# Kernel tuning notes

Hardware: AMD Instinct MI355X
Metric: run time of the kernel (lower is better)

Reference implementation:

```python
import jax, jax.numpy as jnp
import numpy as np

DIM = 384
NUM_HEADS = 12
WS = 7  # window_size
N = WS * WS
BW = 4096  # batch * num_windows


def _relative_position_index(ws: int) -> np.ndarray:
    coords = np.stack(np.meshgrid(np.arange(ws), np.arange(ws), indexing='ij'))  # [2, ws, ws]
    cf = coords.reshape(2, -1)  # [2, ws*ws]
    rel = cf[:, :, None] - cf[:, None, :]  # [2, N, N]
    rel = rel.transpose(1, 2, 0)
    rel[:, :, 0] += ws - 1
    rel[:, :, 1] += ws - 1
    rel[:, :, 0] *= 2 * ws - 1
    return rel.sum(-1).astype(np.int32)  # [N, N]


def setup_inputs() -> dict:
    key = jax.random.key(0)
    ks = jax.random.split(key, 7)
    x = jax.random.normal(ks[0], (BW, N, DIM), dtype=jnp.float32)
    qkv_w = jax.random.normal(ks[1], (3 * DIM, DIM), dtype=jnp.float32) * 0.02
    qkv_b = jnp.zeros((3 * DIM,), dtype=jnp.float32)
    proj_w = jax.random.normal(ks[2], (DIM, DIM), dtype=jnp.float32) * 0.02
    proj_b = jnp.zeros((DIM,), dtype=jnp.float32)
    rpb_table = jax.random.normal(ks[3], ((2 * WS - 1) ** 2, NUM_HEADS), dtype=jnp.float32) * 0.02
    rel_idx = jnp.asarray(_relative_position_index(WS))
    return {"x": x, "qkv_w": qkv_w, "qkv_b": qkv_b, "proj_w": proj_w,
            "proj_b": proj_b, "rpb_table": rpb_table, "rel_idx": rel_idx}


def reference(x, qkv_w, qkv_b, proj_w, proj_b, rpb_table, rel_idx):
    B, n, C = x.shape
    hd = C // NUM_HEADS
    scale = hd ** (-0.5)
    # QKV projection: [B, N, 3C] -> [3, B, H, N, hd]
    qkv = (x @ qkv_w.T + qkv_b).reshape(B, n, 3, NUM_HEADS, hd).transpose(2, 0, 3, 1, 4)
    q, k, v = qkv[0], qkv[1], qkv[2]
    attn = jnp.einsum('bhnd,bhmd->bhnm', q * scale, k)  # [B, H, N, N]
    # relative position bias gather: [N*N, H] -> [H, N, N]
    bias = rpb_table[rel_idx.reshape(-1)].reshape(n, n, NUM_HEADS).transpose(2, 0, 1)
    attn = jax.nn.softmax(attn + bias[None], axis=-1)
    out = jnp.einsum('bhnm,bhmd->bhnd', attn, v).transpose(0, 2, 1, 3).reshape(B, n, C)
    return out @ proj_w.T + proj_b
```

## Files before the change

kernel.cpp:

```cpp
#include <hip/hip_runtime.h>
#include <hip/hip_bf16.h>

typedef __bf16 bf16_t;
typedef __bf16 bf16x8 __attribute__((ext_vector_type(8)));
typedef __bf16 bf16x4 __attribute__((ext_vector_type(4)));
typedef float  f32x4  __attribute__((ext_vector_type(4)));

#define WBT_OFF   0
#define PWB_OFF   (72*12*512*2)
#define BIASL_OFF (PWB_OFF + 24*12*512*2)
#define QKVB_OFF  (BIASL_OFF + 12*4*4*64*4*4)

#define L_HEAD   49152
#define L_HSTR   23040
#define L_O      141312
#define L_TOT    158720

__global__ void prep_kernel(const float* __restrict__ qkv_w,
                            const float* __restrict__ qkv_b,
                            const float* __restrict__ proj_w,
                            const float* __restrict__ rpb,
                            const int*   __restrict__ rel_idx,
                            char* __restrict__ ws)
{
    const int n_wbf  = 72*12*512;
    const int n_pwf  = 24*12*512;
    const int n_bias = 12*4*4*64*4;
    const int n_qb   = 1152;
    int idx = blockIdx.x * blockDim.x + threadIdx.x;
    if (idx < n_wbf) {
        int j = idx & 7, lane = (idx >> 3) & 63;
        int t = idx >> 9;
        int kk = t % 12, ntile = t / 12;
        int lo = lane & 15, hi = lane >> 4;
        int h = ntile / 6, tct = ntile % 6, s = tct >> 1, db = (tct & 1) << 4;
        ((bf16_t*)(ws + WBT_OFF))[idx] =
            (bf16_t)qkv_w[(s*384 + h*32 + db + lo)*384 + kk*32 + hi*8 + j];
    } else if (idx < n_wbf + n_pwf) {
        int li = idx - n_wbf;
        int j = li & 7, lane = (li >> 3) & 63;
        int t = li >> 9;
        int kk = t % 12, ntile = t / 12;
        int lo = lane & 15, hi = lane >> 4;
        ((bf16_t*)(ws + PWB_OFF))[li] =
            (bf16_t)proj_w[(ntile*16 + lo)*384 + kk*32 + hi*8 + j];
    } else if (idx < n_wbf + n_pwf + n_bias) {
        int li = idx - n_wbf - n_pwf;
        int r  = li & 3;
        int l  = (li >> 2) & 63;
        int ct = (li >> 8) & 3;
        int m  = (li >> 10) & 3;
        int h  = li >> 12;
        int i  = m*16 + ((l >> 4) << 2) + r;
        int jj = ct*16 + (l & 15);
        float v;
        if (jj >= 49)     v = -1e30f;
        else if (i < 49)  v = rpb[rel_idx[i*49 + jj]*12 + h];
        else              v = 0.f;
        ((float*)(ws + BIASL_OFF))[li] = v;
    } else if (idx < n_wbf + n_pwf + n_bias + n_qb) {
        int i = idx - n_wbf - n_pwf - n_bias;
        int h = i / 96, c = i % 96;
        int s = c >> 5, cc = c & 31;
        ((float*)(ws + QKVB_OFF))[i] = qkv_b[s*384 + h*32 + cc];
    }
}

__launch_bounds__(512, 2)
__global__ void fused_attn_kernel(const float* __restrict__ x,
                                  const float* __restrict__ proj_b,
                                  const char*  __restrict__ ws,
                                  float* __restrict__ out)
{
    __shared__ __attribute__((aligned(16))) char smem[L_TOT];

    const int tid = threadIdx.x;
    const int lane = tid & 63, lo = lane & 15, hi = lane >> 4;
    const int w = tid >> 6;
    const int wi = blockIdx.x;

    auto xs_addr = [&](int row, int kb) { return row*768 + (kb ^ ((row & 7) << 4)); };

    uint4 z4 = make_uint4(0u,0u,0u,0u);
    for (int c = tid; c < 15*48; c += 512) {
        int row = 49 + c/48, kc = c%48;
        *(uint4*)(smem + xs_addr(row, kc*16)) = z4;
    }
    const float* xw = x + (size_t)wi * (49*384);
    for (int c = tid; c < 49*48; c += 512) {
        int row = c/48, kc = c%48;
        float4 f0 = *(const float4*)(xw + row*384 + kc*8);
        float4 f1 = *(const float4*)(xw + row*384 + kc*8 + 4);
        bf16x8 t;
        t[0]=(bf16_t)f0.x; t[1]=(bf16_t)f0.y; t[2]=(bf16_t)f0.z; t[3]=(bf16_t)f0.w;
        t[4]=(bf16_t)f1.x; t[5]=(bf16_t)f1.y; t[6]=(bf16_t)f1.z; t[7]=(bf16_t)f1.w;
        *(bf16x8*)(smem + xs_addr(row, kc*16)) = t;
    }
    __syncthreads();

    const bf16_t* WBF   = (const bf16_t*)(ws + WBT_OFF);
    const bf16_t* PWF   = (const bf16_t*)(ws + PWB_OFF);
    const float*  biasQ = (const float*)(ws + QKVB_OFF);
    const float scale = 0.17677669529663687f;
    const f32x4 zz = {0.f,0.f,0.f,0.f};

    f32x4 accP[4][3];
#pragma unroll
    for (int m = 0; m < 4; ++m)
#pragma unroll
        for (int nt = 0; nt < 3; ++nt) accP[m][nt] = zz;

    const int hl_a = w >> 1;
    const int mh   = w & 1;
    char* HA = smem + L_HEAD + hl_a*L_HSTR;

#pragma unroll 1
    for (int pass = 0; pass < 3; ++pass) {
        {
            const bf16_t* bb = WBF + (size_t)(pass*8 + w)*(3*12*512) + (lane << 3);
            f32x4 acc[4][3];
#pragma unroll
            for (int m = 0; m < 4; ++m)
#pragma unroll
                for (int nt = 0; nt < 3; ++nt) acc[m][nt] = zz;

            bf16x8 br[3][3];
#pragma unroll
            for (int k = 0; k < 2; ++k)
#pragma unroll
                for (int nt = 0; nt < 3; ++nt)
                    br[k][nt] = *(const bf16x8*)(bb + ((nt*12 + k) << 9));

#pragma unroll
            for (int kk = 0; kk < 12; ++kk) {
                if (kk < 10) {
#pragma unroll
                    for (int nt = 0; nt < 3; ++nt)
                        br[(kk+2)%3][nt] = *(const bf16x8*)(bb + ((nt*12 + kk+2) << 9));
                }
                bf16x8 a[4];
#pragma unroll
                for (int m = 0; m < 4; ++m)
                    a[m] = *(const bf16x8*)(smem + xs_addr(m*16 + lo, kk*64 + hi*16));
#pragma unroll
                for (int nt = 0; nt < 3; ++nt)
#pragma unroll
                    for (int m = 0; m < 4; ++m)
                        acc[m][nt] = __builtin_amdgcn_mfma_f32_16x16x32_bf16(a[m], br[kk%3][nt], acc[m][nt], 0,0,0);
            }

#pragma unroll
            for (int nt = 0; nt < 3; ++nt) {
                const int ntl = w*3 + nt;
                const int hl = ntl / 6, tct = ntl % 6;
                const int s = tct >> 1, db = (tct & 1) << 4;
                float bq = biasQ[(pass*24 + ntl)*16 + lo];
                char* hb = smem + L_HEAD + hl*L_HSTR;
                if (s == 0) {
#pragma unroll
                    for (int m = 0; m < 4; ++m)
#pragma unroll
                        for (int r = 0; r < 4; ++r)
                            *(bf16_t*)(hb + (m*16 + hi*4 + r)*72 + (db + lo)*2) =
                                (bf16_t)((acc[m][nt][r] + bq) * scale);
                } else if (s == 1) {
#pragma unroll
                    for (int m = 0; m < 4; ++m)
#pragma unroll
                        for (int r = 0; r < 4; ++r)
                            *(bf16_t*)(hb + 4608 + (m*16 + hi*4 + r)*72 + (db + lo)*2) =
                                (bf16_t)(acc[m][nt][r] + bq);
                } else {
#pragma unroll
                    for (int m = 0; m < 4; ++m) {
                        bf16x4 p;
#pragma unroll
                        for (int r = 0; r < 4; ++r) p[r] = (bf16_t)(acc[m][nt][r] + bq);
                        *(bf16x4*)(hb + 9216 + (db + lo)*144 + (m*16 + hi*4)*2) = p;
                    }
                }
            }
        }
        __syncthreads();

        {
            const char* QS = HA;
            const char* KS = HA + 4608;
            const char* VT = HA + 9216;
            char*       P  = HA + 13824;
            const float4* bL = (const float4*)(ws + BIASL_OFF) + (size_t)(pass*4 + hl_a)*1024;

            bf16x8 aq[2], bk[4];
#pragma unroll
            for (int mi = 0; mi < 2; ++mi)
                aq[mi] = *(const bf16x8*)(QS + ((mh*2 + mi)*16 + lo)*72 + hi*16);
#pragma unroll
            for (int ct = 0; ct < 4; ++ct)
                bk[ct] = *(const bf16x8*)(KS + (ct*16 + lo)*72 + hi*16);

#pragma unroll
            for (int mi = 0; mi < 2; ++mi) {
                const int m = mh*2 + mi;
                f32x4 s[4];
#pragma unroll
                for (int ct = 0; ct < 4; ++ct) {
                    s[ct] = __builtin_amdgcn_mfma_f32_16x16x32_bf16(aq[mi], bk[ct], zz, 0,0,0);
                    float4 bv = bL[(m*4 + ct)*64 + lane];
                    s[ct][0]+=bv.x; s[ct][1]+=bv.y; s[ct][2]+=bv.z; s[ct][3]+=bv.w;
                }
#pragma unroll
                for (int r = 0; r < 4; ++r) {
                    float mx = fmaxf(fmaxf(s[0][r],s[1][r]), fmaxf(s[2][r],s[3][r]));
#pragma unroll
                    for (int off = 1; off < 16; off <<= 1) mx = fmaxf(mx, __shfl_xor(mx, off));
                    float e0 = __expf(s[0][r]-mx), e1 = __expf(s[1][r]-mx);
                    float e2 = __expf(s[2][r]-mx), e3 = __expf(s[3][r]-mx);
                    float sum = e0+e1+e2+e3;
#pragma unroll
                    for (int off = 1; off < 16; off <<= 1) sum += __shfl_xor(sum, off);
                    float rinv = 1.0f / sum;
                    int row = m*16 + hi*4 + r;
                    *(bf16_t*)(P + row*144 + (0*16+lo)*2) = (bf16_t)(e0*rinv);
                    *(bf16_t*)(P + row*144 + (1*16+lo)*2) = (bf16_t)(e1*rinv);
                    *(bf16_t*)(P + row*144 + (2*16+lo)*2) = (bf16_t)(e2*rinv);
                    *(bf16_t*)(P + row*144 + (3*16+lo)*2) = (bf16_t)(e3*rinv);
                }
            }
            asm volatile("s_waitcnt lgkmcnt(0)" ::: "memory");

#pragma unroll
            for (int mi = 0; mi < 2; ++mi) {
                const int m = mh*2 + mi;
#pragma unroll
                for (int dt = 0; dt < 2; ++dt) {
                    f32x4 o = zz;
#pragma unroll
                    for (int ks = 0; ks < 2; ++ks) {
                        bf16x8 ap = *(const bf16x8*)(P  + (m*16+lo)*144 + ks*64 + hi*16);
                        bf16x8 bv = *(const bf16x8*)(VT + (dt*16+lo)*144 + ks*64 + hi*16);
                        o = __builtin_amdgcn_mfma_f32_16x16x32_bf16(ap, bv, o, 0,0,0);
                    }
                    const int c2 = (hl_a*32 + dt*16 + lo)*2;
#pragma unroll
                    for (int r = 0; r < 4; ++r)
                        *(bf16_t*)(smem + L_O + (m*16 + hi*4 + r)*272 + c2) = (bf16_t)o[r];
                }
            }
        }
        __syncthreads();

        {
            bf16x8 bp[2][3];
#pragma unroll
            for (int nt = 0; nt < 3; ++nt)
                bp[0][nt] = *(const bf16x8*)(PWF + (size_t)(((w*3 + nt)*12 + pass*4) << 9) + (lane << 3));
#pragma unroll
            for (int kk2 = 0; kk2 < 4; ++kk2) {
                if (kk2 < 3) {
#pragma unroll
                    for (int nt = 0; nt < 3; ++nt)
                        bp[(kk2+1)&1][nt] = *(const bf16x8*)(PWF + (size_t)(((w*3 + nt)*12 + pass*4 + kk2+1) << 9) + (lane << 3));
                }
                bf16x8 ao[4];
#pragma unroll
                for (int m = 0; m < 4; ++m)
                    ao[m] = *(const bf16x8*)(smem + L_O + (m*16 + lo)*272 + kk2*64 + hi*16);
#pragma unroll
                for (int nt = 0; nt < 3; ++nt)
#pragma unroll
                    for (int m = 0; m < 4; ++m)
                        accP[m][nt] = __builtin_amdgcn_mfma_f32_16x16x32_bf16(ao[m], bp[kk2&1][nt], accP[m][nt], 0,0,0);
            }
        }
        __syncthreads();
    }

    float* ow = out + (size_t)wi * (49*384);
#pragma unroll
    for (int nt = 0; nt < 3; ++nt) {
        int cc = (w*3 + nt)*16 + lo;
        float pb = proj_b[cc];
#pragma unroll
        for (int m = 0; m < 4; ++m)
#pragma unroll
            for (int r = 0; r < 4; ++r) {
                int row = m*16 + hi*4 + r;
                if (row < 49) ow[row*384 + cc] = accP[m][nt][r] + pb;
            }
    }
}

extern "C" void kernel_launch(void* const* d_in, const int* in_sizes, int n_in,
                              void* d_out, int out_size, void* d_ws, size_t ws_size,
                              hipStream_t stream)
{
    const float* x      = (const float*)d_in[0];
    const float* qkv_w  = (const float*)d_in[1];
    const float* qkv_b  = (const float*)d_in[2];
    const float* proj_w = (const float*)d_in[3];
    const float* proj_b = (const float*)d_in[4];
    const float* rpb    = (const float*)d_in[5];
    const int*   rel_idx= (const int*)d_in[6];
    char* ws = (char*)d_ws;

    const int total = 72*12*512 + 24*12*512 + 12*4*4*64*4 + 1152;
    prep_kernel<<<(total + 255)/256, 256, 0, stream>>>(qkv_w, qkv_b, proj_w, rpb, rel_idx, ws);
    fused_attn_kernel<<<4096, 512, 0, stream>>>(x, proj_b, ws, (float*)d_out);
}
```

Measured before the change: 702.4 us.

## Keep Q and P in registers via transposed MFMA and pipeline proj across passes

Each warp now computes Q, K and V for its own head half with transposed MFMA operands. Q and the softmax probabilities stay in registers and are rearranged with lane shuffles, so they no longer make a round trip through LDS. The output projection for a pass is deferred into the next pass's attention phase with a double-buffered O tile, which removes one block barrier per pass. The aim is to cut LDS traffic and synchronization, at the cost of redundant Q projection work between the paired warps and more register pressure.

Measured after the change: 934.9 us. 33.1% more time.

```diff
diff --git a/kernel.cpp b/kernel.cpp
--- a/kernel.cpp
+++ b/kernel.cpp
@@ -6,18 +6,17 @@
 typedef __bf16 bf16x4 __attribute__((ext_vector_type(4)));
 typedef float  f32x4  __attribute__((ext_vector_type(4)));
 
+#define MFMA __builtin_amdgcn_mfma_f32_16x16x32_bf16
+
 #define WBT_OFF   0
 #define PWB_OFF   (72*12*512*2)
 #define BIASL_OFF (PWB_OFF + 24*12*512*2)
-#define QKVB_OFF  (BIASL_OFF + 12*4*4*64*4*4)
-
-#define L_HEAD   49152
-#define L_HSTR   23040
-#define L_O      141312
-#define L_TOT    158720
+
+#define L_KV   49152
+#define L_OB   (L_KV + 4*9216)
+#define L_TOT  (L_OB + 2*17408)
 
 __global__ void prep_kernel(const float* __restrict__ qkv_w,
-                            const float* __restrict__ qkv_b,
                             const float* __restrict__ proj_w,
                             const float* __restrict__ rpb,
                             const int*   __restrict__ rel_idx,
@@ -26,7 +25,6 @@
     const int n_wbf  = 72*12*512;
     const int n_pwf  = 24*12*512;
     const int n_bias = 12*4*4*64*4;
-    const int n_qb   = 1152;
     int idx = blockIdx.x * blockDim.x + threadIdx.x;
     if (idx < n_wbf) {
         int j = idx & 7, lane = (idx >> 3) & 63;
@@ -48,35 +46,39 @@
         int li = idx - n_wbf - n_pwf;
         int r  = li & 3;
         int l  = (li >> 2) & 63;
-        int ct = (li >> 8) & 3;
-        int m  = (li >> 10) & 3;
+        int kt = (li >> 8) & 3;
+        int mq = (li >> 10) & 3;
         int h  = li >> 12;
-        int i  = m*16 + ((l >> 4) << 2) + r;
-        int jj = ct*16 + (l & 15);
-        float v;
-        if (jj >= 49)     v = -1e30f;
-        else if (i < 49)  v = rpb[rel_idx[i*49 + jj]*12 + h];
-        else              v = 0.f;
+        int q  = mq*16 + (l & 15);
+        int k  = kt*16 + (l >> 4)*4 + r;
+        float v = (k < 49 && q < 49) ? rpb[rel_idx[q*49 + k]*12 + h] : -1e30f;
         ((float*)(ws + BIASL_OFF))[li] = v;
-    } else if (idx < n_wbf + n_pwf + n_bias + n_qb) {
-        int i = idx - n_wbf - n_pwf - n_bias;
-        int h = i / 96, c = i % 96;
-        int s = c >> 5, cc = c & 31;
-        ((float*)(ws + QKVB_OFF))[i] = qkv_b[s*384 + h*32 + cc];
     }
 }
 
+static __device__ __forceinline__ unsigned pack2(float a, float b) {
+    bf16_t xa = (bf16_t)a, xb = (bf16_t)b;
+    unsigned short ua = __builtin_bit_cast(unsigned short, xa);
+    unsigned short ub = __builtin_bit_cast(unsigned short, xb);
+    return (unsigned)ua | ((unsigned)ub << 16);
+}
+
+union U8 { unsigned u[4]; bf16x8 v; };
+
 __launch_bounds__(512, 2)
-__global__ void fused_attn_kernel(const float* __restrict__ x,
-                                  const float* __restrict__ proj_b,
-                                  const char*  __restrict__ ws,
-                                  float* __restrict__ out)
+__global__ void fused2_kernel(const float* __restrict__ x,
+                              const float* __restrict__ qkv_b,
+                              const float* __restrict__ proj_b,
+                              const char*  __restrict__ ws,
+                              float* __restrict__ out)
 {
     __shared__ __attribute__((aligned(16))) char smem[L_TOT];
 
     const int tid = threadIdx.x;
     const int lane = tid & 63, lo = lane & 15, hi = lane >> 4;
     const int w = tid >> 6;
+    const int hl = w >> 1;
+    const int mh = w & 1;
     const int wi = blockIdx.x;
 
     auto xs_addr = [&](int row, int kb) { return row*768 + (kb ^ ((row & 7) << 4)); };
@@ -98,11 +100,12 @@
     }
     __syncthreads();
 
-    const bf16_t* WBF   = (const bf16_t*)(ws + WBT_OFF);
-    const bf16_t* PWF   = (const bf16_t*)(ws + PWB_OFF);
-    const float*  biasQ = (const float*)(ws + QKVB_OFF);
+    const bf16_t* WBF = (const bf16_t*)(ws + WBT_OFF);
+    const bf16_t* PWF = (const bf16_t*)(ws + PWB_OFF);
+    const float4* bT  = (const float4*)(ws + BIASL_OFF);
     const float scale = 0.17677669529663687f;
     const f32x4 zz = {0.f,0.f,0.f,0.f};
+    const int sb = lo + ((hi & 1) << 5);
 
     f32x4 accP[4][3];
 #pragma unroll
@@ -110,169 +113,218 @@
 #pragma unroll
         for (int nt = 0; nt < 3; ++nt) accP[m][nt] = zz;
 
-    const int hl_a = w >> 1;
-    const int mh   = w & 1;
-    char* HA = smem + L_HEAD + hl_a*L_HSTR;
+    bf16x8 bq[2];
 
 #pragma unroll 1
     for (int pass = 0; pass < 3; ++pass) {
+        const int h = pass*4 + hl;
+
         {
-            const bf16_t* bb = WBF + (size_t)(pass*8 + w)*(3*12*512) + (lane << 3);
-            f32x4 acc[4][3];
-#pragma unroll
-            for (int m = 0; m < 4; ++m)
-#pragma unroll
-                for (int nt = 0; nt < 3; ++nt) acc[m][nt] = zz;
-
-            bf16x8 br[3][3];
-#pragma unroll
-            for (int k = 0; k < 2; ++k)
-#pragma unroll
-                for (int nt = 0; nt < 3; ++nt)
-                    br[k][nt] = *(const bf16x8*)(bb + ((nt*12 + k) << 9));
-
+            const bf16_t* wq0b = WBF + (size_t)((h*6 + 0   )*12)*512 + (lane<<3);
+            const bf16_t* wq1b = WBF + (size_t)((h*6 + 1   )*12)*512 + (lane<<3);
+            const bf16_t* wkb  = WBF + (size_t)((h*6 + 2+mh)*12)*512 + (lane<<3);
+            const bf16_t* wvb  = WBF + (size_t)((h*6 + 4+mh)*12)*512 + (lane<<3);
+
+            f32x4 aq[2][2], ak4[4], av4[4];
+#pragma unroll
+            for (int i = 0; i < 2; ++i) { aq[i][0] = zz; aq[i][1] = zz; }
+#pragma unroll
+            for (int i = 0; i < 4; ++i) { ak4[i] = zz; av4[i] = zz; }
+
+            bf16x8 rq0[3], rq1[3], rk[3], rv[3];
+#pragma unroll
+            for (int t = 0; t < 3; ++t) {
+                rq0[t] = *(const bf16x8*)(wq0b + (t<<9));
+                rq1[t] = *(const bf16x8*)(wq1b + (t<<9));
+                rk [t] = *(const bf16x8*)(wkb  + (t<<9));
+                rv [t] = *(const bf16x8*)(wvb  + (t<<9));
+            }
 #pragma unroll
             for (int kk = 0; kk < 12; ++kk) {
-                if (kk < 10) {
-#pragma unroll
-                    for (int nt = 0; nt < 3; ++nt)
-                        br[(kk+2)%3][nt] = *(const bf16x8*)(bb + ((nt*12 + kk+2) << 9));
-                }
-                bf16x8 a[4];
-#pragma unroll
-                for (int m = 0; m < 4; ++m)
-                    a[m] = *(const bf16x8*)(smem + xs_addr(m*16 + lo, kk*64 + hi*16));
-#pragma unroll
-                for (int nt = 0; nt < 3; ++nt)
-#pragma unroll
-                    for (int m = 0; m < 4; ++m)
-                        acc[m][nt] = __builtin_amdgcn_mfma_f32_16x16x32_bf16(a[m], br[kk%3][nt], acc[m][nt], 0,0,0);
-            }
-
-#pragma unroll
-            for (int nt = 0; nt < 3; ++nt) {
-                const int ntl = w*3 + nt;
-                const int hl = ntl / 6, tct = ntl % 6;
-                const int s = tct >> 1, db = (tct & 1) << 4;
-                float bq = biasQ[(pass*24 + ntl)*16 + lo];
-                char* hb = smem + L_HEAD + hl*L_HSTR;
-                if (s == 0) {
-#pragma unroll
-                    for (int m = 0; m < 4; ++m)
-#pragma unroll
-                        for (int r = 0; r < 4; ++r)
-                            *(bf16_t*)(hb + (m*16 + hi*4 + r)*72 + (db + lo)*2) =
-                                (bf16_t)((acc[m][nt][r] + bq) * scale);
-                } else if (s == 1) {
-#pragma unroll
-                    for (int m = 0; m < 4; ++m)
-#pragma unroll
-                        for (int r = 0; r < 4; ++r)
-                            *(bf16_t*)(hb + 4608 + (m*16 + hi*4 + r)*72 + (db + lo)*2) =
-                                (bf16_t)(acc[m][nt][r] + bq);
-                } else {
-#pragma unroll
-                    for (int m = 0; m < 4; ++m) {
-                        bf16x4 p;
-#pragma unroll
-                        for (int r = 0; r < 4; ++r) p[r] = (bf16_t)(acc[m][nt][r] + bq);
-                        *(bf16x4*)(hb + 9216 + (db + lo)*144 + (m*16 + hi*4)*2) = p;
-                    }
-                }
+                const int sl = kk % 3;
+                bf16x8 xf[4];
+#pragma unroll
+                for (int tt = 0; tt < 4; ++tt)
+                    xf[tt] = *(const bf16x8*)(smem + xs_addr(tt*16 + lo, kk*64 + hi*16));
+#pragma unroll
+                for (int mi = 0; mi < 2; ++mi) {
+                    aq[0][mi] = MFMA(rq0[sl], xf[2*mh + mi], aq[0][mi], 0,0,0);
+                    aq[1][mi] = MFMA(rq1[sl], xf[2*mh + mi], aq[1][mi], 0,0,0);
+                }
+#pragma unroll
+                for (int tt = 0; tt < 4; ++tt) ak4[tt] = MFMA(rk[sl], xf[tt], ak4[tt], 0,0,0);
+#pragma unroll
+                for (int tt = 0; tt < 4; ++tt) av4[tt] = MFMA(xf[tt], rv[sl], av4[tt], 0,0,0);
+                if (kk < 9) {
+                    rq0[sl] = *(const bf16x8*)(wq0b + ((kk+3)<<9));
+                    rq1[sl] = *(const bf16x8*)(wq1b + ((kk+3)<<9));
+                    rk [sl] = *(const bf16x8*)(wkb  + ((kk+3)<<9));
+                    rv [sl] = *(const bf16x8*)(wvb  + ((kk+3)<<9));
+                }
+            }
+
+            float4 qb0 = *(const float4*)(qkv_b + h*32 +      hi*4);
+            float4 qb1 = *(const float4*)(qkv_b + h*32 + 16 + hi*4);
+            unsigned pkq[2][2][2];
+#pragma unroll
+            for (int mi = 0; mi < 2; ++mi) {
+                pkq[0][mi][0] = pack2((aq[0][mi][0]+qb0.x)*scale, (aq[0][mi][1]+qb0.y)*scale);
+                pkq[0][mi][1] = pack2((aq[0][mi][2]+qb0.z)*scale, (aq[0][mi][3]+qb0.w)*scale);
+                pkq[1][mi][0] = pack2((aq[1][mi][0]+qb1.x)*scale, (aq[1][mi][1]+qb1.y)*scale);
+                pkq[1][mi][1] = pack2((aq[1][mi][2]+qb1.z)*scale, (aq[1][mi][3]+qb1.w)*scale);
+            }
+#pragma unroll
+            for (int mi = 0; mi < 2; ++mi) {
+                U8 u;
+#pragma unroll
+                for (int jp = 0; jp < 4; ++jp) {
+                    const int rp = jp & 1, hf = jp >> 1;
+                    const int srcl = sb + (hf << 4);
+                    unsigned s0 = (unsigned)__shfl((int)pkq[0][mi][rp], srcl, 64);
+                    unsigned s1 = (unsigned)__shfl((int)pkq[1][mi][rp], srcl, 64);
+                    u.u[jp] = (hi >> 1) ? s1 : s0;
+                }
+                bq[mi] = u.v;
+            }
+
+            float4 kb = *(const float4*)(qkv_b + 384 + h*32 + mh*16 + hi*4);
+            char* Kl = smem + L_KV + hl*9216;
+#pragma unroll
+            for (int tt = 0; tt < 4; ++tt) {
+                bf16x4 t;
+                t[0]=(bf16_t)(ak4[tt][0]+kb.x); t[1]=(bf16_t)(ak4[tt][1]+kb.y);
+                t[2]=(bf16_t)(ak4[tt][2]+kb.z); t[3]=(bf16_t)(ak4[tt][3]+kb.w);
+                *(bf16x4*)(Kl + (tt*16+lo)*72 + (mh*16+hi*4)*2) = t;
+            }
+            float vb = qkv_b[768 + h*32 + mh*16 + lo];
+            char* Vl = Kl + 4608;
+#pragma unroll
+            for (int tt = 0; tt < 4; ++tt) {
+                bf16x4 t;
+                t[0]=(bf16_t)(av4[tt][0]+vb); t[1]=(bf16_t)(av4[tt][1]+vb);
+                t[2]=(bf16_t)(av4[tt][2]+vb); t[3]=(bf16_t)(av4[tt][3]+vb);
+                *(bf16x4*)(Vl + (mh*16+lo)*144 + (tt*16+hi*4)*2) = t;
             }
         }
         __syncthreads();
 
         {
-            const char* QS = HA;
-            const char* KS = HA + 4608;
-            const char* VT = HA + 9216;
-            char*       P  = HA + 13824;
-            const float4* bL = (const float4*)(ws + BIASL_OFF) + (size_t)(pass*4 + hl_a)*1024;
-
-            bf16x8 aq[2], bk[4];
-#pragma unroll
-            for (int mi = 0; mi < 2; ++mi)
-                aq[mi] = *(const bf16x8*)(QS + ((mh*2 + mi)*16 + lo)*72 + hi*16);
-#pragma unroll
-            for (int ct = 0; ct < 4; ++ct)
-                bk[ct] = *(const bf16x8*)(KS + (ct*16 + lo)*72 + hi*16);
-
+            bf16x8 pw[4][3];
+            if (pass > 0) {
+#pragma unroll
+                for (int kk2 = 0; kk2 < 4; ++kk2)
+#pragma unroll
+                    for (int nt = 0; nt < 3; ++nt)
+                        pw[kk2][nt] = *(const bf16x8*)(PWF +
+                            ((size_t)((w*3+nt)*12 + (pass-1)*4 + kk2) << 9) + (lane<<3));
+            }
+
+            const char* Kl = smem + L_KV + hl*9216;
+            const char* Vl = Kl + 4608;
+            bf16x8 akf[4];
+#pragma unroll
+            for (int kt = 0; kt < 4; ++kt)
+                akf[kt] = *(const bf16x8*)(Kl + (kt*16+lo)*72 + hi*16);
+            bf16x8 avf[2][2];
+#pragma unroll
+            for (int dt = 0; dt < 2; ++dt)
+#pragma unroll
+                for (int ks = 0; ks < 2; ++ks)
+                    avf[dt][ks] = *(const bf16x8*)(Vl + (dt*16+lo)*144 + ks*64 + hi*16);
+
+            char* Ob = smem + L_OB + (pass & 1)*17408;
 #pragma unroll
             for (int mi = 0; mi < 2; ++mi) {
-                const int m = mh*2 + mi;
-                f32x4 s[4];
-#pragma unroll
-                for (int ct = 0; ct < 4; ++ct) {
-                    s[ct] = __builtin_amdgcn_mfma_f32_16x16x32_bf16(aq[mi], bk[ct], zz, 0,0,0);
-                    float4 bv = bL[(m*4 + ct)*64 + lane];
-                    s[ct][0]+=bv.x; s[ct][1]+=bv.y; s[ct][2]+=bv.z; s[ct][3]+=bv.w;
-                }
-#pragma unroll
-                for (int r = 0; r < 4; ++r) {
-                    float mx = fmaxf(fmaxf(s[0][r],s[1][r]), fmaxf(s[2][r],s[3][r]));
-#pragma unroll
-                    for (int off = 1; off < 16; off <<= 1) mx = fmaxf(mx, __shfl_xor(mx, off));
-                    float e0 = __expf(s[0][r]-mx), e1 = __expf(s[1][r]-mx);
-                    float e2 = __expf(s[2][r]-mx), e3 = __expf(s[3][r]-mx);
-                    float sum = e0+e1+e2+e3;
-#pragma unroll
-                    for (int off = 1; off < 16; off <<= 1) sum += __shfl_xor(sum, off);
-                    float rinv = 1.0f / sum;
-                    int row = m*16 + hi*4 + r;
-                    *(bf16_t*)(P + row*144 + (0*16+lo)*2) = (bf16_t)(e0*rinv);
-                    *(bf16_t*)(P + row*144 + (1*16+lo)*2) = (bf16_t)(e1*rinv);
-                    *(bf16_t*)(P + row*144 + (2*16+lo)*2) = (bf16_t)(e2*rinv);
-                    *(bf16_t*)(P + row*144 + (3*16+lo)*2) = (bf16_t)(e3*rinv);
-                }
-            }
-            asm volatile("s_waitcnt lgkmcnt(0)" ::: "memory");
-
-#pragma unroll
-            for (int mi = 0; mi < 2; ++mi) {
-                const int m = mh*2 + mi;
+                const int mq = mh*2 + mi;
+                f32x4 st[4];
+#pragma unroll
+                for (int kt = 0; kt < 4; ++kt) {
+                    st[kt] = MFMA(akf[kt], bq[mi], zz, 0,0,0);
+                    float4 bv = bT[((h*4 + mq)*4 + kt)*64 + lane];
+                    st[kt][0]+=bv.x; st[kt][1]+=bv.y; st[kt][2]+=bv.z; st[kt][3]+=bv.w;
+                }
+                float mx = fmaxf(fmaxf(fmaxf(st[0][0],st[0][1]), fmaxf(st[0][2],st[0][3])),
+                                 fmaxf(fmaxf(st[1][0],st[1][1]), fmaxf(st[1][2],st[1][3])));
+                mx = fmaxf(mx, fmaxf(fmaxf(fmaxf(st[2][0],st[2][1]), fmaxf(st[2][2],st[2][3])),
+                                     fmaxf(fmaxf(st[3][0],st[3][1]), fmaxf(st[3][2],st[3][3]))));
+                mx = fmaxf(mx, __shfl_xor(mx, 16));
+                mx = fmaxf(mx, __shfl_xor(mx, 32));
+                float e[4][4]; float sum = 0.f;
+#pragma unroll
+                for (int kt = 0; kt < 4; ++kt)
+#pragma unroll
+                    for (int r = 0; r < 4; ++r) { e[kt][r] = __expf(st[kt][r] - mx); sum += e[kt][r]; }
+                sum += __shfl_xor(sum, 16);
+                sum += __shfl_xor(sum, 32);
+                float rinv = 1.0f / sum;
+                unsigned pkp[4][2];
+#pragma unroll
+                for (int kt = 0; kt < 4; ++kt) {
+                    pkp[kt][0] = pack2(e[kt][0]*rinv, e[kt][1]*rinv);
+                    pkp[kt][1] = pack2(e[kt][2]*rinv, e[kt][3]*rinv);
+                }
+                bf16x8 bp[2];
+#pragma unroll
+                for (int ks = 0; ks < 2; ++ks) {
+                    U8 u;
+#pragma unroll
+                    for (int jp = 0; jp < 4; ++jp) {
+                        const int rp = jp & 1, hf = jp >> 1;
+                        const int srcl = sb + (hf << 4);
+                        unsigned s0 = (unsigned)__shfl((int)pkp[2*ks  ][rp], srcl, 64);
+                        unsigned s1 = (unsigned)__shfl((int)pkp[2*ks+1][rp], srcl, 64);
+                        u.u[jp] = (hi >> 1) ? s1 : s0;
+                    }
+                    bp[ks] = u.v;
+                }
 #pragma unroll
                 for (int dt = 0; dt < 2; ++dt) {
-                    f32x4 o = zz;
-#pragma unroll
-                    for (int ks = 0; ks < 2; ++ks) {
-                        bf16x8 ap = *(const bf16x8*)(P  + (m*16+lo)*144 + ks*64 + hi*16);
-                        bf16x8 bv = *(const bf16x8*)(VT + (dt*16+lo)*144 + ks*64 + hi*16);
-                        o = __builtin_amdgcn_mfma_f32_16x16x32_bf16(ap, bv, o, 0,0,0);
-                    }
-                    const int c2 = (hl_a*32 + dt*16 + lo)*2;
-#pragma unroll
-                    for (int r = 0; r < 4; ++r)
-                        *(bf16_t*)(smem + L_O + (m*16 + hi*4 + r)*272 + c2) = (bf16_t)o[r];
+                    f32x4 o = MFMA(avf[dt][0], bp[0], zz, 0,0,0);
+                    o = MFMA(avf[dt][1], bp[1], o, 0,0,0);
+                    bf16x4 t;
+                    t[0]=(bf16_t)o[0]; t[1]=(bf16_t)o[1]; t[2]=(bf16_t)o[2]; t[3]=(bf16_t)o[3];
+                    *(bf16x4*)(Ob + (mq*16+lo)*272 + (hl*32 + dt*16 + hi*4)*2) = t;
+                }
+            }
+
+            if (pass > 0) {
+                const char* Op = smem + L_OB + ((pass-1) & 1)*17408;
+#pragma unroll
+                for (int kk2 = 0; kk2 < 4; ++kk2) {
+                    bf16x8 ao[4];
+#pragma unroll
+                    for (int m = 0; m < 4; ++m)
+                        ao[m] = *(const bf16x8*)(Op + (m*16+lo)*272 + kk2*64 + hi*16);
+#pragma unroll
+                    for (int nt = 0; nt < 3; ++nt)
+#pragma unroll
+                        for (int m = 0; m < 4; ++m)
+                            accP[m][nt] = MFMA(ao[m], pw[kk2][nt], accP[m][nt], 0,0,0);
                 }
             }
         }
         __syncthreads();
-
-        {
-            bf16x8 bp[2][3];
+    }
+
+    {
+        const char* Op = smem + L_OB;
+#pragma unroll
+        for (int kk2 = 0; kk2 < 4; ++kk2) {
+            bf16x8 pb2[3];
 #pragma unroll
             for (int nt = 0; nt < 3; ++nt)
-                bp[0][nt] = *(const bf16x8*)(PWF + (size_t)(((w*3 + nt)*12 + pass*4) << 9) + (lane << 3));
-#pragma unroll
-            for (int kk2 = 0; kk2 < 4; ++kk2) {
-                if (kk2 < 3) {
-#pragma unroll
-                    for (int nt = 0; nt < 3; ++nt)
-                        bp[(kk2+1)&1][nt] = *(const bf16x8*)(PWF + (size_t)(((w*3 + nt)*12 + pass*4 + kk2+1) << 9) + (lane << 3));
-                }
-                bf16x8 ao[4];
+                pb2[nt] = *(const bf16x8*)(PWF +
+                    ((size_t)((w*3+nt)*12 + 8 + kk2) << 9) + (lane<<3));
+            bf16x8 ao[4];
+#pragma unroll
+            for (int m = 0; m < 4; ++m)
+                ao[m] = *(const bf16x8*)(Op + (m*16+lo)*272 + kk2*64 + hi*16);
+#pragma unroll
+            for (int nt = 0; nt < 3; ++nt)
 #pragma unroll
                 for (int m = 0; m < 4; ++m)
-                    ao[m] = *(const bf16x8*)(smem + L_O + (m*16 + lo)*272 + kk2*64 + hi*16);
-#pragma unroll
-                for (int nt = 0; nt < 3; ++nt)
-#pragma unroll
-                    for (int m = 0; m < 4; ++m)
-                        accP[m][nt] = __builtin_amdgcn_mfma_f32_16x16x32_bf16(ao[m], bp[kk2&1][nt], accP[m][nt], 0,0,0);
-            }
+                    accP[m][nt] = MFMA(ao[m], pb2[nt], accP[m][nt], 0,0,0);
         }
-        __syncthreads();
     }
 
     float* ow = out + (size_t)wi * (49*384);
@@ -303,7 +355,7 @@
     const int*   rel_idx= (const int*)d_in[6];
     char* ws = (char*)d_ws;
 
-    const int total = 72*12*512 + 24*12*512 + 12*4*4*64*4 + 1152;
-    prep_kernel<<<(total + 255)/256, 256, 0, stream>>>(qkv_w, qkv_b, proj_w, rpb, rel_idx, ws);
-    fused_attn_kernel<<<4096, 512, 0, stream>>>(x, proj_b, ws, (float*)d_out);
+    const int total = 72*12*512 + 24*12*512 + 12*4*4*64*4;
+    prep_kernel<<<(total + 255)/256, 256, 0, stream>>>(qkv_w, proj_w, rpb, rel_idx, ws);
+    fused2_kernel<<<4096, 512, 0, stream>>>(x, qkv_b, proj_b, ws, (float*)d_out);
 }
```

## Compute transposed attention scores and pass softmax probabilities via lane shuffles

Applied to the files above, without the earlier changes.

Swaps operands in the QK MFMA so scores come out transposed, letting the per-query softmax reduce mostly within registers and only two cross-lane shuffles. The normalized probabilities are packed to bf16 and redistributed with shuffles directly into MFMA operand layout, eliminating the P buffer in shared memory and its store/load round trip. The bias table layout is regenerated to match, LDS footprint shrinks, and one end-of-pass barrier is removed, which relies on region disjointness for correctness.

Result: faster. 665.1 us (-5.3%).

```diff
diff --git a/kernel.cpp b/kernel.cpp
--- a/kernel.cpp
+++ b/kernel.cpp
@@ -6,15 +6,17 @@
 typedef __bf16 bf16x4 __attribute__((ext_vector_type(4)));
 typedef float  f32x4  __attribute__((ext_vector_type(4)));
 
+#define MFMA __builtin_amdgcn_mfma_f32_16x16x32_bf16
+
 #define WBT_OFF   0
 #define PWB_OFF   (72*12*512*2)
 #define BIASL_OFF (PWB_OFF + 24*12*512*2)
 #define QKVB_OFF  (BIASL_OFF + 12*4*4*64*4*4)
 
 #define L_HEAD   49152
-#define L_HSTR   23040
-#define L_O      141312
-#define L_TOT    158720
+#define L_HSTR   13824
+#define L_O      104448
+#define L_TOT    121856
 
 __global__ void prep_kernel(const float* __restrict__ qkv_w,
                             const float* __restrict__ qkv_b,
@@ -48,15 +50,12 @@
         int li = idx - n_wbf - n_pwf;
         int r  = li & 3;
         int l  = (li >> 2) & 63;
-        int ct = (li >> 8) & 3;
-        int m  = (li >> 10) & 3;
+        int kt = (li >> 8) & 3;
+        int mq = (li >> 10) & 3;
         int h  = li >> 12;
-        int i  = m*16 + ((l >> 4) << 2) + r;
-        int jj = ct*16 + (l & 15);
-        float v;
-        if (jj >= 49)     v = -1e30f;
-        else if (i < 49)  v = rpb[rel_idx[i*49 + jj]*12 + h];
-        else              v = 0.f;
+        int q  = mq*16 + (l & 15);
+        int k  = kt*16 + (l >> 4)*4 + r;
+        float v = (k < 49 && q < 49) ? rpb[rel_idx[q*49 + k]*12 + h] : -1e30f;
         ((float*)(ws + BIASL_OFF))[li] = v;
     } else if (idx < n_wbf + n_pwf + n_bias + n_qb) {
         int i = idx - n_wbf - n_pwf - n_bias;
@@ -66,11 +65,20 @@
     }
 }
 
+static __device__ __forceinline__ unsigned pack2(float a, float b) {
+    bf16_t xa = (bf16_t)a, xb = (bf16_t)b;
+    unsigned short ua = __builtin_bit_cast(unsigned short, xa);
+    unsigned short ub = __builtin_bit_cast(unsigned short, xb);
+    return (unsigned)ua | ((unsigned)ub << 16);
+}
+
+union U8 { unsigned u[4]; bf16x8 v; };
+
 __launch_bounds__(512, 2)
-__global__ void fused_attn_kernel(const float* __restrict__ x,
-                                  const float* __restrict__ proj_b,
-                                  const char*  __restrict__ ws,
-                                  float* __restrict__ out)
+__global__ void fused4_kernel(const float* __restrict__ x,
+                              const float* __restrict__ proj_b,
+                              const char*  __restrict__ ws,
+                              float* __restrict__ out)
 {
     __shared__ __attribute__((aligned(16))) char smem[L_TOT];
 
@@ -100,9 +108,11 @@
 
     const bf16_t* WBF   = (const bf16_t*)(ws + WBT_OFF);
     const bf16_t* PWF   = (const bf16_t*)(ws + PWB_OFF);
+    const float4* bT    = (const float4*)(ws + BIASL_OFF);
     const float*  biasQ = (const float*)(ws + QKVB_OFF);
     const float scale = 0.17677669529663687f;
     const f32x4 zz = {0.f,0.f,0.f,0.f};
+    const int sb = lo + ((hi & 1) << 5);
 
     f32x4 accP[4][3];
 #pragma unroll
@@ -112,7 +122,6 @@
 
     const int hl_a = w >> 1;
     const int mh   = w & 1;
-    char* HA = smem + L_HEAD + hl_a*L_HSTR;
 
 #pragma unroll 1
     for (int pass = 0; pass < 3; ++pass) {
@@ -146,7 +155,7 @@
                 for (int nt = 0; nt < 3; ++nt)
 #pragma unroll
                     for (int m = 0; m < 4; ++m)
-                        acc[m][nt] = __builtin_amdgcn_mfma_f32_16x16x32_bf16(a[m], br[kk%3][nt], acc[m][nt], 0,0,0);
+                        acc[m][nt] = MFMA(a[m], br[kk%3][nt], acc[m][nt], 0,0,0);
             }
 
 #pragma unroll
@@ -184,82 +193,87 @@
         __syncthreads();
 
         {
-            const char* QS = HA;
-            const char* KS = HA + 4608;
-            const char* VT = HA + 9216;
-            char*       P  = HA + 13824;
-            const float4* bL = (const float4*)(ws + BIASL_OFF) + (size_t)(pass*4 + hl_a)*1024;
-
-            bf16x8 aq[2], bk[4];
-#pragma unroll
-            for (int mi = 0; mi < 2; ++mi)
-                aq[mi] = *(const bf16x8*)(QS + ((mh*2 + mi)*16 + lo)*72 + hi*16);
-#pragma unroll
-            for (int ct = 0; ct < 4; ++ct)
-                bk[ct] = *(const bf16x8*)(KS + (ct*16 + lo)*72 + hi*16);
+            const int h = pass*4 + hl_a;
+            const char* Ql = smem + L_HEAD + hl_a*L_HSTR;
+            const char* Kl = Ql + 4608;
+            const char* Vl = Ql + 9216;
+            char* Ob = smem + L_O;
+
+            bf16x8 akf[4];
+#pragma unroll
+            for (int kt = 0; kt < 4; ++kt)
+                akf[kt] = *(const bf16x8*)(Kl + (kt*16+lo)*72 + hi*16);
 
 #pragma unroll
             for (int mi = 0; mi < 2; ++mi) {
-                const int m = mh*2 + mi;
-                f32x4 s[4];
-#pragma unroll
-                for (int ct = 0; ct < 4; ++ct) {
-                    s[ct] = __builtin_amdgcn_mfma_f32_16x16x32_bf16(aq[mi], bk[ct], zz, 0,0,0);
-                    float4 bv = bL[(m*4 + ct)*64 + lane];
-                    s[ct][0]+=bv.x; s[ct][1]+=bv.y; s[ct][2]+=bv.z; s[ct][3]+=bv.w;
-                }
-#pragma unroll
-                for (int r = 0; r < 4; ++r) {
-                    float mx = fmaxf(fmaxf(s[0][r],s[1][r]), fmaxf(s[2][r],s[3][r]));
-#pragma unroll
-                    for (int off = 1; off < 16; off <<= 1) mx = fmaxf(mx, __shfl_xor(mx, off));
-                    float e0 = __expf(s[0][r]-mx), e1 = __expf(s[1][r]-mx);
-                    float e2 = __expf(s[2][r]-mx), e3 = __expf(s[3][r]-mx);
-                    float sum = e0+e1+e2+e3;
-#pragma unroll
-                    for (int off = 1; off < 16; off <<= 1) sum += __shfl_xor(sum, off);
-                    float rinv = 1.0f / sum;
-                    int row = m*16 + hi*4 + r;
-                    *(bf16_t*)(P + row*144 + (0*16+lo)*2) = (bf16_t)(e0*rinv);
-                    *(bf16_t*)(P + row*144 + (1*16+lo)*2) = (bf16_t)(e1*rinv);
-                    *(bf16_t*)(P + row*144 + (2*16+lo)*2) = (bf16_t)(e2*rinv);
-                    *(bf16_t*)(P + row*144 + (3*16+lo)*2) = (bf16_t)(e3*rinv);
-                }
-            }
-            asm volatile("s_waitcnt lgkmcnt(0)" ::: "memory");
-
-#pragma unroll
-            for (int mi = 0; mi < 2; ++mi) {
-                const int m = mh*2 + mi;
+                const int mq = mh*2 + mi;
+                bf16x8 qf = *(const bf16x8*)(Ql + (mq*16+lo)*72 + hi*16);
+                f32x4 st[4];
+#pragma unroll
+                for (int kt = 0; kt < 4; ++kt) {
+                    st[kt] = MFMA(akf[kt], qf, zz, 0,0,0);
+                    float4 bv = bT[((h*4 + mq)*4 + kt)*64 + lane];
+                    st[kt][0]+=bv.x; st[kt][1]+=bv.y; st[kt][2]+=bv.z; st[kt][3]+=bv.w;
+                }
+                float mx = fmaxf(fmaxf(fmaxf(st[0][0],st[0][1]), fmaxf(st[0][2],st[0][3])),
+                                 fmaxf(fmaxf(st[1][0],st[1][1]), fmaxf(st[1][2],st[1][3])));
+                mx = fmaxf(mx, fmaxf(fmaxf(fmaxf(st[2][0],st[2][1]), fmaxf(st[2][2],st[2][3])),
+                                     fmaxf(fmaxf(st[3][0],st[3][1]), fmaxf(st[3][2],st[3][3]))));
+                mx = fmaxf(mx, __shfl_xor(mx, 16));
+                mx = fmaxf(mx, __shfl_xor(mx, 32));
+                float sum = 0.f;
+#pragma unroll
+                for (int kt = 0; kt < 4; ++kt)
+#pragma unroll
+                    for (int r = 0; r < 4; ++r) { st[kt][r] = __expf(st[kt][r] - mx); sum += st[kt][r]; }
+                sum += __shfl_xor(sum, 16);
+                sum += __shfl_xor(sum, 32);
+                float rinv = 1.0f / sum;
+                unsigned pkp[4][2];
+#pragma unroll
+                for (int kt = 0; kt < 4; ++kt) {
+                    pkp[kt][0] = pack2(st[kt][0]*rinv, st[kt][1]*rinv);
+                    pkp[kt][1] = pack2(st[kt][2]*rinv, st[kt][3]*rinv);
+                }
+                bf16x8 bp[2];
+#pragma unroll
+                for (int ks = 0; ks < 2; ++ks) {
+                    U8 u;
+#pragma unroll
+                    for (int jp = 0; jp < 4; ++jp) {
+                        const int rp = jp & 1, hf = jp >> 1;
+                        const int srcl = sb + (hf << 4);
+                        unsigned s0 = (unsigned)__shfl((int)pkp[2*ks  ][rp], srcl, 64);
+                        unsigned s1 = (unsigned)__shfl((int)pkp[2*ks+1][rp], srcl, 64);
+                        u.u[jp] = (hi >> 1) ? s1 : s0;
+                    }
+                    bp[ks] = u.v;
+                }
 #pragma unroll
                 for (int dt = 0; dt < 2; ++dt) {
-                    f32x4 o = zz;
-#pragma unroll
-                    for (int ks = 0; ks < 2; ++ks) {
-                        bf16x8 ap = *(const bf16x8*)(P  + (m*16+lo)*144 + ks*64 + hi*16);
-                        bf16x8 bv = *(const bf16x8*)(VT + (dt*16+lo)*144 + ks*64 + hi*16);
-                        o = __builtin_amdgcn_mfma_f32_16x16x32_bf16(ap, bv, o, 0,0,0);
-                    }
-                    const int c2 = (hl_a*32 + dt*16 + lo)*2;
-#pragma unroll
-                    for (int r = 0; r < 4; ++r)
-                        *(bf16_t*)(smem + L_O + (m*16 + hi*4 + r)*272 + c2) = (bf16_t)o[r];
+                    bf16x8 av0 = *(const bf16x8*)(Vl + (dt*16+lo)*144 +      hi*16);
+                    bf16x8 av1 = *(const bf16x8*)(Vl + (dt*16+lo)*144 + 64 + hi*16);
+                    f32x4 o = MFMA(av0, bp[0], zz, 0,0,0);
+                    o = MFMA(av1, bp[1], o, 0,0,0);
+                    bf16x4 t;
+                    t[0]=(bf16_t)o[0]; t[1]=(bf16_t)o[1]; t[2]=(bf16_t)o[2]; t[3]=(bf16_t)o[3];
+                    *(bf16x4*)(Ob + (mq*16+lo)*272 + (hl_a*32 + dt*16 + hi*4)*2) = t;
                 }
             }
         }
         __syncthreads();
 
         {
-            bf16x8 bp[2][3];
+            bf16x8 pj[2][3];
 #pragma unroll
             for (int nt = 0; nt < 3; ++nt)
-                bp[0][nt] = *(const bf16x8*)(PWF + (size_t)(((w*3 + nt)*12 + pass*4) << 9) + (lane << 3));
+                pj[0][nt] = *(const bf16x8*)(PWF + ((size_t)((w*3+nt)*12 + pass*4) << 9) + (lane<<3));
 #pragma unroll
             for (int kk2 = 0; kk2 < 4; ++kk2) {
                 if (kk2 < 3) {
 #pragma unroll
                     for (int nt = 0; nt < 3; ++nt)
-                        bp[(kk2+1)&1][nt] = *(const bf16x8*)(PWF + (size_t)(((w*3 + nt)*12 + pass*4 + kk2+1) << 9) + (lane << 3));
+                        pj[(kk2+1)&1][nt] = *(const bf16x8*)(PWF + ((size_t)((w*3+nt)*12 + pass*4 + kk2+1) << 9) + (lane<<3));
                 }
                 bf16x8 ao[4];
 #pragma unroll
@@ -269,10 +283,9 @@
                 for (int nt = 0; nt < 3; ++nt)
 #pragma unroll
                     for (int m = 0; m < 4; ++m)
-                        accP[m][nt] = __builtin_amdgcn_mfma_f32_16x16x32_bf16(ao[m], bp[kk2&1][nt], accP[m][nt], 0,0,0);
+                        accP[m][nt] = MFMA(ao[m], pj[kk2&1][nt], accP[m][nt], 0,0,0);
             }
         }
-        __syncthreads();
     }
 
     float* ow = out + (size_t)wi * (49*384);
@@ -305,5 +318,5 @@
 
     const int total = 72*12*512 + 24*12*512 + 12*4*4*64*4 + 1152;
     prep_kernel<<<(total + 255)/256, 256, 0, stream>>>(qkv_w, qkv_b, proj_w, rpb, rel_idx, ws);
-    fused_attn_kernel<<<4096, 512, 0, stream>>>(x, proj_b, ws, (float*)d_out);
+    fused4_kernel<<<4096, 512, 0, stream>>>(x, proj_b, ws, (float*)d_out);
 }
```
